# Performance work log

Measured on AMD Instinct MI355X. Metric: run time of the kernel, lower is better.

Reference implementation:

```python
import jax, jax.numpy as jnp
import numpy as np

N = 250000
E = 8000000
G = 1024  # num graphs
F_IN = 16
H = 9
EPS_BN = 1e-5


def gat_conv(x, edge_index, W, att_src, att_dst, bias):
    # PyG GATConv (heads=1, add_self_loops=True, negative_slope=0.2)
    h = x @ W                               # [N, H]
    src = jnp.concatenate([edge_index[0], jnp.arange(N)])  # self-loops
    dst = jnp.concatenate([edge_index[1], jnp.arange(N)])
    a_src = h @ att_src                     # [N]
    a_dst = h @ att_dst                     # [N]
    e = jax.nn.leaky_relu(a_src[src] + a_dst[dst], 0.2)    # [E+N]
    m = jax.lax.stop_gradient(jax.ops.segment_max(e, dst, num_segments=N))
    ex = jnp.exp(e - m[dst])
    s = jax.ops.segment_sum(ex, dst, num_segments=N)
    alpha = ex / (s[dst] + 1e-16)
    out = jax.ops.segment_sum(h[src] * alpha[:, None], dst, num_segments=N)
    return out + bias


def batch_norm(x, gamma, beta):
    mu = x.mean(0)
    var = x.var(0)  # biased, as PyTorch uses for normalization
    return gamma * (x - mu) * jax.lax.rsqrt(var + EPS_BN) + beta


def setup_inputs() -> dict:
    key = jax.random.key(0)
    ks = jax.random.split(key, 20)
    x = jax.random.normal(ks[0], (N, F_IN), dtype=jnp.float32)
    edge_index = jax.random.randint(ks[1], (2, E), 0, N, dtype=jnp.int64)
    batch = jnp.sort(jax.random.randint(ks[2], (N,), 0, G, dtype=jnp.int64))
    p = {}
    p['W1'] = jax.random.normal(ks[3], (F_IN, H), dtype=jnp.float32) * 0.3
    p['as1'] = jax.random.normal(ks[4], (H,), dtype=jnp.float32) * 0.3
    p['ad1'] = jax.random.normal(ks[5], (H,), dtype=jnp.float32) * 0.3
    p['b1'] = jnp.zeros((H,), dtype=jnp.float32)
    p['g1'] = jnp.ones((H,), dtype=jnp.float32)
    p['be1'] = jnp.zeros((H,), dtype=jnp.float32)
    p['W2'] = jax.random.normal(ks[6], (H, H), dtype=jnp.float32) * 0.3
    p['as2'] = jax.random.normal(ks[7], (H,), dtype=jnp.float32) * 0.3
    p['ad2'] = jax.random.normal(ks[8], (H,), dtype=jnp.float32) * 0.3
    p['b2'] = jnp.zeros((H,), dtype=jnp.float32)
    p['g2'] = jnp.ones((H,), dtype=jnp.float32)
    p['be2'] = jnp.zeros((H,), dtype=jnp.float32)
    for i, (di, do) in enumerate([(H, H), (H, H), (H, H), (H, 1)], start=1):
        p[f'mW{i}'] = jax.random.normal(ks[8 + 2 * i], (di, do), dtype=jnp.float32) * 0.3
        p[f'mb{i}'] = jnp.zeros((do,), dtype=jnp.float32)
    return {'x': x, 'edge_index': edge_index, 'batch': batch, **p}


def reference(x, edge_index, batch, W1, as1, ad1, b1, g1, be1,
              W2, as2, ad2, b2, g2, be2,
              mW1, mb1, mW2, mb2, mW3, mb3, mW4, mb4):
    h = gat_conv(x, edge_index, W1, as1, ad1, b1)
    h = jax.nn.relu(h)
    h = batch_norm(h, g1, be1)
    # dropout is identity at inference
    h = gat_conv(h, edge_index, W2, as2, ad2, b2)
    h = jax.nn.relu(h)
    h = batch_norm(h, g2, be2)
    pooled = jax.ops.segment_sum(h, batch, num_segments=G)  # [G, H]
    o = pooled @ mW1 + mb1
    o = o @ mW2 + mb2
    o = o @ mW3 + mb3
    o = o @ mW4 + mb4
    return o
```

## Files before the change

kernel.cpp:

```cpp
#include <hip/hip_runtime.h>

#define NN 250000
#define NE 8000000
#define NG 1024
#define FIN 16
#define HD 9
#define NSTAGE 64

#define CBIN 1024
#define NPB 245
#define NBK 1024
#define EPB 7813
#define LOFFW 1025
#define SCAP 9216

static __device__ __forceinline__ float lrelu(float v) { return v > 0.f ? v : 0.2f * v; }

static __device__ __forceinline__ unsigned f2bf(float f) {
    unsigned u = __float_as_uint(f);
    return (u + 0x7fffu + ((u >> 16) & 1u)) >> 16;
}
static __device__ __forceinline__ float bf_lo(unsigned u) { return __uint_as_float(u << 16); }
static __device__ __forceinline__ float bf_hi(unsigned u) { return __uint_as_float(u & 0xffff0000u); }

static __device__ __forceinline__ int block_excl_scan(int v, int* total)
{
    int lane = threadIdx.x & 63, wv = threadIdx.x >> 6;
    int ps = v;
#pragma unroll
    for (int o = 1; o < 64; o <<= 1) { int u = __shfl_up(ps, o); if (lane >= o) ps += u; }
    __shared__ int wsum[4];
    if (lane == 63) wsum[wv] = ps;
    __syncthreads();
    int woff = 0;
    for (int w = 0; w < wv; w++) woff += wsum[w];
    if (total) *total = wsum[0] + wsum[1] + wsum[2] + wsum[3];
    __syncthreads();
    return woff + ps - v;
}

__global__ void __launch_bounds__(256) chunk_sort(
    const int* __restrict__ srcs, const int* __restrict__ dsts,
    int* __restrict__ schunk, int* __restrict__ lrow)
{
    __shared__ int hist[CBIN];
    __shared__ int stage[EPB];
    int t = threadIdx.x, b = blockIdx.x;
    int base = b * EPB;
    int end = base + EPB; if (end > NE) end = NE;
    int n = end - base;
    for (int c = t; c < CBIN; c += 256) hist[c] = 0;
    __syncthreads();
    for (int e = base + t; e < end; e += 256)
        atomicAdd(&hist[(unsigned)dsts[e] / NPB], 1);
    __syncthreads();
    int v0 = hist[4*t], v1 = hist[4*t+1], v2 = hist[4*t+2], v3 = hist[4*t+3];
    int ex = block_excl_scan(v0 + v1 + v2 + v3, nullptr);
    int e0 = ex, e1 = ex + v0, e2 = e1 + v1, e3 = e2 + v2;
    hist[4*t] = e0; hist[4*t+1] = e1; hist[4*t+2] = e2; hist[4*t+3] = e3;
    int* lr = lrow + (size_t)b * LOFFW;
    lr[4*t] = e0; lr[4*t+1] = e1; lr[4*t+2] = e2; lr[4*t+3] = e3;
    if (t == 255) lr[CBIN] = n;
    __syncthreads();
    for (int e = base + t; e < end; e += 256) {
        int src = srcs[e], dst = dsts[e];
        int bin = (unsigned)dst / NPB;
        int p = atomicAdd(&hist[bin], 1);
        stage[p] = (src << 8) | (dst - bin * NPB);
    }
    __syncthreads();
    for (int i = t; i < n; i += 256) schunk[base + i] = stage[i];
}

__global__ void __launch_bounds__(256) bin_scan_chunks(
    const int* __restrict__ lrow, int* __restrict__ chunkoff, int* __restrict__ bintot)
{
    int bin = blockIdx.x, t = threadIdx.x;
    int v[4]; int sum = 0;
#pragma unroll
    for (int j = 0; j < 4; j++) {
        const int* lr = lrow + (size_t)(4 * t + j) * LOFFW + bin;
        v[j] = lr[1] - lr[0];
        sum += v[j];
    }
    int tot;
    int ex = block_excl_scan(sum, &tot);
    int run = ex;
#pragma unroll
    for (int j = 0; j < 4; j++) {
        chunkoff[(size_t)(4 * t + j) * CBIN + bin] = run;
        run += v[j];
    }
    if (t == 0) bintot[bin] = tot;
}

__global__ void __launch_bounds__(256) bin_scan_bins(const int* __restrict__ bintot, int* __restrict__ binbase)
{
    int t = threadIdx.x;
    int i0 = 4 * t;
    int v0 = bintot[i0], v1 = bintot[i0 + 1], v2 = bintot[i0 + 2], v3 = bintot[i0 + 3];
    int ex = block_excl_scan(v0 + v1 + v2 + v3, nullptr);
    binbase[i0] = ex; binbase[i0 + 1] = ex + v0;
    binbase[i0 + 2] = ex + v0 + v1; binbase[i0 + 3] = ex + v0 + v1 + v2;
    if (t == 255) binbase[CBIN] = ex + v0 + v1 + v2 + v3;
}

__global__ void __launch_bounds__(256) place_copy(
    const int* __restrict__ schunk, const int* __restrict__ lrow,
    const int* __restrict__ chunkoff, const int* __restrict__ binbase,
    int* __restrict__ binned)
{
    int t = threadIdx.x, c = blockIdx.x;
    size_t base = (size_t)c * EPB;
    const int* lr = lrow + (size_t)c * LOFFW;
    for (int b = t; b < CBIN; b += 256) {
        int lo = lr[b], hi = lr[b + 1];
        size_t g = (size_t)binbase[b] + chunkoff[(size_t)c * CBIN + b];
        for (int i = lo; i < hi; i++) binned[g + (i - lo)] = schunk[base + i];
    }
}

__global__ void __launch_bounds__(256) bin_sort(
    int* __restrict__ binned, const int* __restrict__ binbase, int* __restrict__ off)
{
    __shared__ int cntS[256];
    __shared__ int stage[SCAP];
    int bin = blockIdx.x, t = threadIdx.x;
    int beg = binbase[bin], end = binbase[bin + 1];
    cntS[t] = 0;
    __syncthreads();
    for (int i = beg + t; i < end; i += 256)
        atomicAdd(&cntS[binned[i] & 255], 1);
    __syncthreads();
    int ex = block_excl_scan(cntS[t], nullptr);
    int node = bin * NPB + t;
    if (t < NPB && node <= NN) off[node] = beg + ex;
    cntS[t] = ex;
    __syncthreads();
    for (int i = beg + t; i < end; i += 256) {
        int rec = binned[i];
        int p = atomicAdd(&cntS[rec & 255], 1);
        if (p < SCAP) stage[p] = rec >> 8;
    }
    __syncthreads();
    int n = end - beg; if (n > SCAP) n = SCAP;
    for (int i = t; i < n; i += 256) binned[beg + i] = stage[i];
}

__global__ void __launch_bounds__(256) node_prep1(
    const float* __restrict__ x, const float* __restrict__ W,
    const float* __restrict__ as_, const float* __restrict__ ad_,
    uint2* __restrict__ hq, float* __restrict__ adst,
    float* __restrict__ s, float* __restrict__ acc)
{
    __shared__ float sW[FIN * HD];
    __shared__ float sas[HD], sad[HD];
    for (int t = threadIdx.x; t < FIN * HD; t += 256) sW[t] = W[t];
    if (threadIdx.x < HD) { sas[threadIdx.x] = as_[threadIdx.x]; sad[threadIdx.x] = ad_[threadIdx.x]; }
    __syncthreads();
    int i = blockIdx.x * 256 + threadIdx.x;
    if (i >= NN) return;
    float xi[FIN];
    const float4* xp = reinterpret_cast<const float4*>(x + (size_t)i * FIN);
#pragma unroll
    for (int q = 0; q < 4; q++) { float4 v = xp[q]; xi[4*q] = v.x; xi[4*q+1] = v.y; xi[4*q+2] = v.z; xi[4*q+3] = v.w; }
    float hv[HD];
#pragma unroll
    for (int k = 0; k < HD; k++) {
        float a = 0.f;
#pragma unroll
        for (int j = 0; j < FIN; j++) a = fmaf(xi[j], sW[j * HD + k], a);
        hv[k] = a;
    }
    float sa = 0.f, sd = 0.f;
#pragma unroll
    for (int k = 0; k < HD; k++) { sa = fmaf(hv[k], sas[k], sa); sd = fmaf(hv[k], sad[k], sd); }
    float w = __expf(lrelu(sa + sd));
    adst[i] = sd; s[i] = w;
    uint2* hp = hq + (size_t)i * 3;
    hp[0] = make_uint2(f2bf(hv[0]) | (f2bf(hv[1]) << 16), f2bf(hv[2]) | (f2bf(hv[3]) << 16));
    hp[1] = make_uint2(f2bf(hv[4]) | (f2bf(hv[5]) << 16), f2bf(hv[6]) | (f2bf(hv[7]) << 16));
    hp[2] = make_uint2(f2bf(hv[8]), __float_as_uint(sa));
#pragma unroll
    for (int k = 0; k < HD; k++) acc[(size_t)i*HD+k] = w * hv[k];
}

__global__ void __launch_bounds__(256) node_prep2(
    const float* __restrict__ accin, const float* __restrict__ sin, const float* __restrict__ b,
    const float* __restrict__ sc, const float* __restrict__ sh,
    const float* __restrict__ W, const float* __restrict__ as_, const float* __restrict__ ad_,
    uint2* __restrict__ hq, float* __restrict__ adst,
    float* __restrict__ s, float* __restrict__ acc)
{
    __shared__ float sW[HD * HD];
    __shared__ float sas[HD], sad[HD], ssc[HD], ssh[HD], sb[HD];
    for (int t = threadIdx.x; t < HD * HD; t += 256) sW[t] = W[t];
    if (threadIdx.x < HD) {
        sas[threadIdx.x] = as_[threadIdx.x]; sad[threadIdx.x] = ad_[threadIdx.x];
        ssc[threadIdx.x] = sc[threadIdx.x]; ssh[threadIdx.x] = sh[threadIdx.x];
        sb[threadIdx.x] = b[threadIdx.x];
    }
    __syncthreads();
    int i = blockIdx.x * 256 + threadIdx.x;
    if (i >= NN) return;
    float inv = 1.0f / (sin[i] + 1e-16f);
    float xi[HD];
#pragma unroll
    for (int k = 0; k < HD; k++) {
        float v = fmaf(accin[(size_t)i*HD+k], inv, sb[k]);
        v = v > 0.f ? v : 0.f;
        xi[k] = fmaf(v, ssc[k], ssh[k]);
    }
    float hv[HD];
#pragma unroll
    for (int k = 0; k < HD; k++) {
        float a = 0.f;
#pragma unroll
        for (int j = 0; j < HD; j++) a = fmaf(xi[j], sW[j * HD + k], a);
        hv[k] = a;
    }
    float sa = 0.f, sd = 0.f;
#pragma unroll
    for (int k = 0; k < HD; k++) { sa = fmaf(hv[k], sas[k], sa); sd = fmaf(hv[k], sad[k], sd); }
    float w = __expf(lrelu(sa + sd));
    adst[i] = sd; s[i] = w;
    uint2* hp = hq + (size_t)i * 3;
    hp[0] = make_uint2(f2bf(hv[0]) | (f2bf(hv[1]) << 16), f2bf(hv[2]) | (f2bf(hv[3]) << 16));
    hp[1] = make_uint2(f2bf(hv[4]) | (f2bf(hv[5]) << 16), f2bf(hv[6]) | (f2bf(hv[7]) << 16));
    hp[2] = make_uint2(f2bf(hv[8]), __float_as_uint(sa));
#pragma unroll
    for (int k = 0; k < HD; k++) acc[(size_t)i*HD+k] = w * hv[k];
}

#define ACCUM(w, A, B, C) \
    a[0] = fmaf(w, bf_lo(A.x), a[0]); a[1] = fmaf(w, bf_hi(A.x), a[1]); \
    a[2] = fmaf(w, bf_lo(A.y), a[2]); a[3] = fmaf(w, bf_hi(A.y), a[3]); \
    a[4] = fmaf(w, bf_lo(B.x), a[4]); a[5] = fmaf(w, bf_hi(B.x), a[5]); \
    a[6] = fmaf(w, bf_lo(B.y), a[6]); a[7] = fmaf(w, bf_hi(B.y), a[7]); \
    a[8] = fmaf(w, bf_lo(C.x), a[8]);

__global__ void __launch_bounds__(256) gat_gather(
    const int* __restrict__ off, const int* __restrict__ esrc,
    const uint2* __restrict__ hq, const float* __restrict__ adst,
    float* __restrict__ s, float* __restrict__ acc)
{
    int gidx = blockIdx.x * 32 + (threadIdx.x >> 3);
    int lane = threadIdx.x & 7;
    if (gidx >= NN) return;
    int beg = off[gidx], end = off[gidx + 1];
    float ad = adst[gidx];
    float wsum = 0.f;
    float a[HD];
#pragma unroll
    for (int k = 0; k < HD; k++) a[k] = 0.f;
    int e = beg + lane;
    for (; e + 8 < end; e += 16) {
        int s0 = esrc[e], s1 = esrc[e + 8];
        const uint2* p0 = hq + (size_t)s0 * 3;
        const uint2* p1 = hq + (size_t)s1 * 3;
        uint2 A0 = p0[0], B0 = p0[1], C0 = p0[2];
        uint2 A1 = p1[0], B1 = p1[1], C1 = p1[2];
        float w0 = __expf(lrelu(__uint_as_float(C0.y) + ad));
        float w1 = __expf(lrelu(__uint_as_float(C1.y) + ad));
        wsum += w0 + w1;
        ACCUM(w0, A0, B0, C0);
        ACCUM(w1, A1, B1, C1);
    }
    if (e < end) {
        int s0 = esrc[e];
        const uint2* p0 = hq + (size_t)s0 * 3;
        uint2 A0 = p0[0], B0 = p0[1], C0 = p0[2];
        float w0 = __expf(lrelu(__uint_as_float(C0.y) + ad));
        wsum += w0;
        ACCUM(w0, A0, B0, C0);
    }
#pragma unroll
    for (int o = 1; o < 8; o <<= 1) {
        wsum += __shfl_xor(wsum, o);
#pragma unroll
        for (int k = 0; k < HD; k++) a[k] += __shfl_xor(a[k], o);
    }
    if (lane == 0) {
        s[gidx] += wsum;
        float* ap = acc + (size_t)gidx * HD;
#pragma unroll
        for (int k = 0; k < HD; k++) ap[k] += a[k];
    }
}

__global__ void __launch_bounds__(256) node_finish1(
    const float* __restrict__ acc, const float* __restrict__ s, const float* __restrict__ b,
    float* __restrict__ stage)
{
    int i = blockIdx.x * 256 + threadIdx.x;
    bool act = i < NN;
    float inv = act ? 1.0f / (s[i] + 1e-16f) : 0.f;
    float y[HD];
#pragma unroll
    for (int k = 0; k < HD; k++) {
        float v = act ? fmaf(acc[(size_t)i*HD+k], inv, __ldg(&b[k])) : 0.f;
        y[k] = v > 0.f ? v : 0.f;
    }
    __shared__ float red[4][2 * HD];
    int lane = threadIdx.x & 63, wv = threadIdx.x >> 6;
#pragma unroll
    for (int k = 0; k < HD; k++) {
        float sm = y[k], sq = y[k] * y[k];
#pragma unroll
        for (int o = 32; o > 0; o >>= 1) { sm += __shfl_down(sm, o); sq += __shfl_down(sq, o); }
        if (lane == 0) { red[wv][k] = sm; red[wv][HD + k] = sq; }
    }
    __syncthreads();
    int t = threadIdx.x;
    if (t < 2 * HD) {
        float v = red[0][t] + red[1][t] + red[2][t] + red[3][t];
        atomicAdd(&stage[(blockIdx.x & (NSTAGE - 1)) * 2 * HD + t], v);
    }
}

__global__ void __launch_bounds__(256) node_finish2(
    const float* __restrict__ acc, const float* __restrict__ s, const float* __restrict__ b,
    const int* __restrict__ batch,
    float* __restrict__ stage,
    float* __restrict__ pool, float* __restrict__ cnt)
{
    int i = blockIdx.x * 256 + threadIdx.x;
    bool act = i < NN;
    float inv = act ? 1.0f / (s[i] + 1e-16f) : 0.f;
    float y[HD];
#pragma unroll
    for (int k = 0; k < HD; k++) {
        float v = act ? fmaf(acc[(size_t)i*HD+k], inv, __ldg(&b[k])) : 0.f;
        y[k] = v > 0.f ? v : 0.f;
    }
    __shared__ float red[4][2 * HD];
    int lane = threadIdx.x & 63, wv = threadIdx.x >> 6;
#pragma unroll
    for (int k = 0; k < HD; k++) {
        float sm = y[k], sq = y[k] * y[k];
#pragma unroll
        for (int o = 32; o > 0; o >>= 1) { sm += __shfl_down(sm, o); sq += __shfl_down(sq, o); }
        if (lane == 0) { red[wv][k] = sm; red[wv][HD + k] = sq; }
    }
    __syncthreads();
    int t = threadIdx.x;
    if (t < 2 * HD) {
        float v = red[0][t] + red[1][t] + red[2][t] + red[3][t];
        atomicAdd(&stage[(blockIdx.x & (NSTAGE - 1)) * 2 * HD + t], v);
    }
    int g = act ? batch[i] : -1;
    unsigned long long alive = __ballot(g >= 0);
    while (alive) {
        int leader = (int)__builtin_ctzll(alive);
        int g0 = __shfl(g, leader);
        bool mine = (g == g0);
#pragma unroll
        for (int k = 0; k < HD; k++) {
            float v = mine ? y[k] : 0.f;
#pragma unroll
            for (int o = 32; o > 0; o >>= 1) v += __shfl_xor(v, o);
            if (lane == leader) atomicAdd(&pool[g0 * HD + k], v);
        }
        float c = mine ? 1.f : 0.f;
#pragma unroll
        for (int o = 32; o > 0; o >>= 1) c += __shfl_xor(c, o);
        if (lane == leader) atomicAdd(&cnt[g0], c);
        alive &= ~__ballot(mine);
    }
}

__global__ void bn_finalize(const float* __restrict__ stage,
                            const float* __restrict__ gamma, const float* __restrict__ beta,
                            float* __restrict__ scale, float* __restrict__ shift)
{
    __shared__ float tot[2 * HD];
    int t = threadIdx.x;
    if (t < 2 * HD) {
        float v = 0.f;
        for (int j = 0; j < NSTAGE; j++) v += stage[j * 2 * HD + t];
        tot[t] = v;
    }
    __syncthreads();
    if (t < HD) {
        float mu = tot[t] * (1.0f / NN);
        float var = tot[HD + t] * (1.0f / NN) - mu * mu;
        float rstd = rsqrtf(var + 1e-5f);
        float sc = gamma[t] * rstd;
        scale[t] = sc;
        shift[t] = beta[t] - mu * sc;
    }
}

__global__ void __launch_bounds__(256) final_mlp(
    const float* __restrict__ pool, const float* __restrict__ cnt,
    const float* __restrict__ sc, const float* __restrict__ sh,
    const float* __restrict__ mW1, const float* __restrict__ mb1,
    const float* __restrict__ mW2, const float* __restrict__ mb2,
    const float* __restrict__ mW3, const float* __restrict__ mb3,
    const float* __restrict__ mW4, const float* __restrict__ mb4,
    float* __restrict__ out)
{
    __shared__ float w1[81], w2[81], w3[81], bb1[9], bb2[9], bb3[9], w4[9], ssc[9], ssh[9];
    int t = threadIdx.x;
    if (t < 81) { w1[t] = mW1[t]; w2[t] = mW2[t]; w3[t] = mW3[t]; }
    if (t < 9) {
        bb1[t] = mb1[t]; bb2[t] = mb2[t]; bb3[t] = mb3[t];
        w4[t] = mW4[t]; ssc[t] = sc[t]; ssh[t] = sh[t];
    }
    __syncthreads();
    int g = blockIdx.x * 256 + t;
    if (g >= NG) return;
    float c = cnt[g];
    float p[9], q[9];
#pragma unroll
    for (int k = 0; k < 9; k++) p[k] = fmaf(ssc[k], pool[g * 9 + k], ssh[k] * c);
#pragma unroll
    for (int k = 0; k < 9; k++) {
        float a = bb1[k];
#pragma unroll
        for (int j = 0; j < 9; j++) a = fmaf(p[j], w1[j * 9 + k], a);
        q[k] = a;
    }
#pragma unroll
    for (int k = 0; k < 9; k++) {
        float a = bb2[k];
#pragma unroll
        for (int j = 0; j < 9; j++) a = fmaf(q[j], w2[j * 9 + k], a);
        p[k] = a;
    }
#pragma unroll
    for (int k = 0; k < 9; k++) {
        float a = bb3[k];
#pragma unroll
        for (int j = 0; j < 9; j++) a = fmaf(p[j], w3[j * 9 + k], a);
        q[k] = a;
    }
    float o = mb4[0];
#pragma unroll
    for (int j = 0; j < 9; j++) o = fmaf(q[j], w4[j], o);
    out[g] = o;
}

extern "C" void kernel_launch(void* const* d_in, const int* in_sizes, int n_in,
                              void* d_out, int out_size, void* d_ws, size_t ws_size,
                              hipStream_t stream)
{
    const float* x   = (const float*)d_in[0];
    const int*   ei  = (const int*)d_in[1];
    const int*   bat = (const int*)d_in[2];
    const float* W1  = (const float*)d_in[3];
    const float* as1 = (const float*)d_in[4];
    const float* ad1 = (const float*)d_in[5];
    const float* b1  = (const float*)d_in[6];
    const float* g1  = (const float*)d_in[7];
    const float* be1 = (const float*)d_in[8];
    const float* W2  = (const float*)d_in[9];
    const float* as2 = (const float*)d_in[10];
    const float* ad2 = (const float*)d_in[11];
    const float* b2  = (const float*)d_in[12];
    const float* g2  = (const float*)d_in[13];
    const float* be2 = (const float*)d_in[14];
    const float* mW1 = (const float*)d_in[15];
    const float* mb1 = (const float*)d_in[16];
    const float* mW2 = (const float*)d_in[17];
    const float* mb2 = (const float*)d_in[18];
    const float* mW3 = (const float*)d_in[19];
    const float* mb3 = (const float*)d_in[20];
    const float* mW4 = (const float*)d_in[21];
    const float* mb4 = (const float*)d_in[22];
    float* out = (float*)d_out;

    float* ws   = (float*)d_ws;
    float* zb   = ws;
    float* stg1 = zb;
    float* stg2 = stg1 + NSTAGE * 2 * HD;
    float* pool = stg2 + NSTAGE * 2 * HD;
    float* cnt  = pool + (size_t)NG * HD;
    float* sc1  = cnt + NG;
    float* sh1  = sc1 + HD;
    float* sc2  = sh1 + HD;
    float* sh2  = sc2 + HD;
    int*   off    = (int*)(sh2 + HD);
    int*   binned = off + (NN + 1);
    int*   uni    = binned + NE;
    int*   schunk = uni;
    uint2* hq     = (uint2*)uni;
    float* adst   = (float*)uni + (size_t)NN * 6;
    float* s      = adst + NN;
    float* acc    = s + NN;
    int*   lrow     = uni + NE;
    int*   chunkoff = lrow + (size_t)NBK * LOFFW;
    int*   bintot   = chunkoff + (size_t)NBK * CBIN;
    int*   binbase  = bintot + CBIN;

    size_t zbytes = (size_t)(2 * NSTAGE * 2 * HD + NG * HD + NG + 4 * HD) * sizeof(float);
    hipMemsetAsync(zb, 0, zbytes, stream);

    const int* srcs = ei;
    const int* dsts = ei + NE;
    int nb  = (NN + 255) / 256;
    int ngb = (NN + 31) / 32;

    chunk_sort<<<NBK, 256, 0, stream>>>(srcs, dsts, schunk, lrow);
    bin_scan_chunks<<<CBIN, 256, 0, stream>>>(lrow, chunkoff, bintot);
    bin_scan_bins<<<1, 256, 0, stream>>>(bintot, binbase);
    place_copy<<<NBK, 256, 0, stream>>>(schunk, lrow, chunkoff, binbase, binned);
    bin_sort<<<CBIN, 256, 0, stream>>>(binned, binbase, off);

    node_prep1<<<nb, 256, 0, stream>>>(x, W1, as1, ad1, hq, adst, s, acc);
    gat_gather<<<ngb, 256, 0, stream>>>(off, binned, hq, adst, s, acc);
    node_finish1<<<nb, 256, 0, stream>>>(acc, s, b1, stg1);
    bn_finalize<<<1, 64, 0, stream>>>(stg1, g1, be1, sc1, sh1);

    node_prep2<<<nb, 256, 0, stream>>>(acc, s, b1, sc1, sh1, W2, as2, ad2, hq, adst, s, acc);
    gat_gather<<<ngb, 256, 0, stream>>>(off, binned, hq, adst, s, acc);
    node_finish2<<<nb, 256, 0, stream>>>(acc, s, b2, bat, stg2, pool, cnt);
    bn_finalize<<<1, 64, 0, stream>>>(stg2, g2, be2, sc2, sh2);

    final_mlp<<<(NG + 255) / 256, 256, 0, stream>>>(pool, cnt, sc2, sh2,
                                                    mW1, mb1, mW2, mb2, mW3, mb3, mW4, mb4, out);
}
```

Before: 350.1 us.

## Fuse bin placement into per-bin sort and unroll gather loop to four edges

Merges place_copy and bin_sort into one bin_build kernel. Each bin block pulls its segments straight from every chunk into shared memory using transposed offset and start tables, then sorts locally by destination node, which removes one full global write and read of the edge records and one kernel launch. In exchange, shared memory per block doubles to two staging arrays, which may lower occupancy, and each thread copies uncoalesced short runs from 1024 chunks. The gather loop is also unrolled from two to four edges per iteration, with a loop tail, to keep more independent loads in flight at some cost in registers.

```diff
diff --git a/kernel.cpp b/kernel.cpp
--- a/kernel.cpp
+++ b/kernel.cpp
@@ -73,25 +73,31 @@
 }
 
 __global__ void __launch_bounds__(256) bin_scan_chunks(
-    const int* __restrict__ lrow, int* __restrict__ chunkoff, int* __restrict__ bintot)
+    const int* __restrict__ lrow, int* __restrict__ coffT, int* __restrict__ rstartT,
+    int* __restrict__ bintot)
 {
     int bin = blockIdx.x, t = threadIdx.x;
-    int v[4]; int sum = 0;
+    int v[4], st[4]; int sum = 0;
 #pragma unroll
     for (int j = 0; j < 4; j++) {
         const int* lr = lrow + (size_t)(4 * t + j) * LOFFW + bin;
+        st[j] = lr[0];
         v[j] = lr[1] - lr[0];
         sum += v[j];
     }
     int tot;
     int ex = block_excl_scan(sum, &tot);
     int run = ex;
+    int* co = coffT + (size_t)bin * (NBK + 1);
+    int* rs = rstartT + (size_t)bin * NBK;
 #pragma unroll
     for (int j = 0; j < 4; j++) {
-        chunkoff[(size_t)(4 * t + j) * CBIN + bin] = run;
+        co[4 * t + j] = run;
+        rs[4 * t + j] = st[j];
         run += v[j];
     }
     if (t == 0) bintot[bin] = tot;
+    if (t == 255) co[NBK] = run;
 }
 
 __global__ void __launch_bounds__(256) bin_scan_bins(const int* __restrict__ bintot, int* __restrict__ binbase)
@@ -105,46 +111,41 @@
     if (t == 255) binbase[CBIN] = ex + v0 + v1 + v2 + v3;
 }
 
-__global__ void __launch_bounds__(256) place_copy(
-    const int* __restrict__ schunk, const int* __restrict__ lrow,
-    const int* __restrict__ chunkoff, const int* __restrict__ binbase,
-    int* __restrict__ binned)
-{
-    int t = threadIdx.x, c = blockIdx.x;
-    size_t base = (size_t)c * EPB;
-    const int* lr = lrow + (size_t)c * LOFFW;
-    for (int b = t; b < CBIN; b += 256) {
-        int lo = lr[b], hi = lr[b + 1];
-        size_t g = (size_t)binbase[b] + chunkoff[(size_t)c * CBIN + b];
-        for (int i = lo; i < hi; i++) binned[g + (i - lo)] = schunk[base + i];
-    }
-}
-
-__global__ void __launch_bounds__(256) bin_sort(
-    int* __restrict__ binned, const int* __restrict__ binbase, int* __restrict__ off)
-{
+__global__ void __launch_bounds__(256) bin_build(
+    const int* __restrict__ schunk, const int* __restrict__ coffT, const int* __restrict__ rstartT,
+    const int* __restrict__ binbase, int* __restrict__ binned, int* __restrict__ off)
+{
+    __shared__ int stageA[SCAP];
+    __shared__ int stageB[SCAP];
     __shared__ int cntS[256];
-    __shared__ int stage[SCAP];
     int bin = blockIdx.x, t = threadIdx.x;
-    int beg = binbase[bin], end = binbase[bin + 1];
+    int beg = binbase[bin];
+    int n = binbase[bin + 1] - beg; if (n > SCAP) n = SCAP;
+    const int* co = coffT + (size_t)bin * (NBK + 1);
+    const int* rs = rstartT + (size_t)bin * NBK;
+    for (int c = t; c < NBK; c += 256) {
+        int o = co[c], len = co[c + 1] - o;
+        const int* sp = schunk + (size_t)c * EPB + rs[c];
+        for (int j = 0; j < len; j++)
+            if (o + j < SCAP) stageA[o + j] = sp[j];
+    }
     cntS[t] = 0;
     __syncthreads();
-    for (int i = beg + t; i < end; i += 256)
-        atomicAdd(&cntS[binned[i] & 255], 1);
+    for (int i = t; i < n; i += 256)
+        atomicAdd(&cntS[stageA[i] & 255], 1);
     __syncthreads();
     int ex = block_excl_scan(cntS[t], nullptr);
     int node = bin * NPB + t;
     if (t < NPB && node <= NN) off[node] = beg + ex;
     cntS[t] = ex;
     __syncthreads();
-    for (int i = beg + t; i < end; i += 256) {
-        int rec = binned[i];
+    for (int i = t; i < n; i += 256) {
+        int rec = stageA[i];
         int p = atomicAdd(&cntS[rec & 255], 1);
-        if (p < SCAP) stage[p] = rec >> 8;
-    }
-    __syncthreads();
-    int n = end - beg; if (n > SCAP) n = SCAP;
-    for (int i = t; i < n; i += 256) binned[beg + i] = stage[i];
+        if (p < SCAP) stageB[p] = rec >> 8;
+    }
+    __syncthreads();
+    for (int i = t; i < n; i += 256) binned[beg + i] = stageB[i];
 }
 
 __global__ void __launch_bounds__(256) node_prep1(
@@ -254,19 +255,27 @@
 #pragma unroll
     for (int k = 0; k < HD; k++) a[k] = 0.f;
     int e = beg + lane;
-    for (; e + 8 < end; e += 16) {
-        int s0 = esrc[e], s1 = esrc[e + 8];
+    for (; e + 24 < end; e += 32) {
+        int s0 = esrc[e], s1 = esrc[e + 8], s2 = esrc[e + 16], s3 = esrc[e + 24];
         const uint2* p0 = hq + (size_t)s0 * 3;
         const uint2* p1 = hq + (size_t)s1 * 3;
+        const uint2* p2 = hq + (size_t)s2 * 3;
+        const uint2* p3 = hq + (size_t)s3 * 3;
         uint2 A0 = p0[0], B0 = p0[1], C0 = p0[2];
         uint2 A1 = p1[0], B1 = p1[1], C1 = p1[2];
+        uint2 A2 = p2[0], B2 = p2[1], C2 = p2[2];
+        uint2 A3 = p3[0], B3 = p3[1], C3 = p3[2];
         float w0 = __expf(lrelu(__uint_as_float(C0.y) + ad));
         float w1 = __expf(lrelu(__uint_as_float(C1.y) + ad));
-        wsum += w0 + w1;
+        float w2 = __expf(lrelu(__uint_as_float(C2.y) + ad));
+        float w3 = __expf(lrelu(__uint_as_float(C3.y) + ad));
+        wsum += (w0 + w1) + (w2 + w3);
         ACCUM(w0, A0, B0, C0);
         ACCUM(w1, A1, B1, C1);
-    }
-    if (e < end) {
+        ACCUM(w2, A2, B2, C2);
+        ACCUM(w3, A3, B3, C3);
+    }
+    for (; e < end; e += 8) {
         int s0 = esrc[e];
         const uint2* p0 = hq + (size_t)s0 * 3;
         uint2 A0 = p0[0], B0 = p0[1], C0 = p0[2];
@@ -488,10 +497,11 @@
     float* adst   = (float*)uni + (size_t)NN * 6;
     float* s      = adst + NN;
     float* acc    = s + NN;
-    int*   lrow     = uni + NE;
-    int*   chunkoff = lrow + (size_t)NBK * LOFFW;
-    int*   bintot   = chunkoff + (size_t)NBK * CBIN;
-    int*   binbase  = bintot + CBIN;
+    int*   lrow    = uni + NE;
+    int*   coffT   = lrow + (size_t)NBK * LOFFW;
+    int*   rstartT = coffT + (size_t)CBIN * (NBK + 1);
+    int*   bintot  = rstartT + (size_t)CBIN * NBK;
+    int*   binbase = bintot + CBIN;
 
     size_t zbytes = (size_t)(2 * NSTAGE * 2 * HD + NG * HD + NG + 4 * HD) * sizeof(float);
     hipMemsetAsync(zb, 0, zbytes, stream);
@@ -502,10 +512,9 @@
     int ngb = (NN + 31) / 32;
 
     chunk_sort<<<NBK, 256, 0, stream>>>(srcs, dsts, schunk, lrow);
-    bin_scan_chunks<<<CBIN, 256, 0, stream>>>(lrow, chunkoff, bintot);
+    bin_scan_chunks<<<CBIN, 256, 0, stream>>>(lrow, coffT, rstartT, bintot);
     bin_scan_bins<<<1, 256, 0, stream>>>(bintot, binbase);
-    place_copy<<<NBK, 256, 0, stream>>>(schunk, lrow, chunkoff, binbase, binned);
-    bin_sort<<<CBIN, 256, 0, stream>>>(binned, binbase, off);
+    bin_build<<<CBIN, 256, 0, stream>>>(schunk, coffT, rstartT, binbase, binned, off);
 
     node_prep1<<<nb, 256, 0, stream>>>(x, W1, as1, ad1, hq, adst, s, acc);
     gat_gather<<<ngb, 256, 0, stream>>>(off, binned, hq, adst, s, acc);
```

Result: slower. 394.4 us (+12.7%).
